# Kernel tuning notes

Hardware: AMD Instinct MI355X
Metric: run time of the kernel (lower is better)

Reference implementation:

```python
import jax, jax.numpy as jnp
import numpy as np

GRAPH_SIZE = 1024
D_MODEL = 256
BATCH = 32
INITIAL_ALPHA = 1.0


def setup_inputs() -> dict:
    key = jax.random.key(0)
    ks = jax.random.split(key, 10)
    s = 1.0 / np.sqrt(D_MODEL)  # torch Linear default init scale
    inp = {
        "query": jax.random.normal(ks[0], (BATCH, GRAPH_SIZE, D_MODEL), jnp.float32),
        "key_": jax.random.normal(ks[1], (BATCH, GRAPH_SIZE, D_MODEL), jnp.float32),
        "value": jax.random.normal(ks[2], (BATCH, GRAPH_SIZE, D_MODEL), jnp.float32),
        "dist": jax.random.uniform(ks[3], (BATCH, GRAPH_SIZE, GRAPH_SIZE), jnp.float32),
        "Wq": jax.random.uniform(ks[4], (D_MODEL, D_MODEL), jnp.float32, -s, s),
        "bq": jax.random.uniform(ks[5], (D_MODEL,), jnp.float32, -s, s),
        "Wk": jax.random.uniform(ks[6], (D_MODEL, D_MODEL), jnp.float32, -s, s),
        "bk": jax.random.uniform(ks[7], (D_MODEL,), jnp.float32, -s, s),
        "Wv": jax.random.uniform(ks[8], (D_MODEL, D_MODEL), jnp.float32, -s, s),
        "bv": jax.random.uniform(ks[9], (D_MODEL,), jnp.float32, -s, s),
        # alpha_raw = exp(initial_alpha - 1)
        "alpha_raw": jnp.asarray(np.exp(INITIAL_ALPHA - 1.0), jnp.float32),
    }
    return inp


def reference(query, key_, value, dist, Wq, bq, Wk, bk, Wv, bv, alpha_raw):
    # self-attention path: mask=None, cross=False, query_size == graph_size
    log2_N = jnp.log2(jnp.asarray(GRAPH_SIZE, jnp.float32))
    alpha = jax.nn.softplus(alpha_raw) + 1e-6

    q = jnp.einsum('bnd,ed->bne', query, Wq) + bq   # fc_q
    k = jnp.einsum('bnd,ed->bne', key_, Wk) + bk    # fc_k
    v = jnp.einsum('bnd,ed->bne', value, Wv) + bv   # fc_v

    exp_A = jnp.exp(-alpha * log2_N * dist)         # [b, n, n]
    exp_K = jnp.exp(k)                              # [b, n, d]

    numerator = jnp.einsum('bqk,bkd->bqd', exp_A, exp_K * v)
    denominator = jnp.einsum('bqk,bkd->bqd', exp_A, exp_K) + 1e-8
    return jax.nn.sigmoid(q) * (numerator / denominator)
```

## Files before the change

### kernel.cpp

```cpp
#include <hip/hip_runtime.h>
#include <hip/hip_bf16.h>

#define NBATCH 32
#define NG 1024
#define DM 256
#define HB 16

typedef short bf16x8 __attribute__((ext_vector_type(8)));
typedef float f32x4 __attribute__((ext_vector_type(4)));
typedef unsigned short u16x4 __attribute__((ext_vector_type(4)));
typedef unsigned short u16x8 __attribute__((ext_vector_type(8)));

static __device__ __forceinline__ unsigned short f2bf(float f) {
    __hip_bfloat16 h = __float2bfloat16(f);
    return *reinterpret_cast<unsigned short*>(&h);
}

static __device__ __forceinline__ void gload16(const void* g, void* l) {
    __builtin_amdgcn_global_load_lds(
        (const __attribute__((address_space(1))) unsigned int*)g,
        (__attribute__((address_space(3))) unsigned int*)l, 16, 0, 0);
}

__global__ __launch_bounds__(256) void wpack_kernel(
    const float* __restrict__ Wq, const float* __restrict__ Wk,
    const float* __restrict__ Wv, unsigned short* __restrict__ Wb)
{
    const int i4 = (blockIdx.x * 256 + threadIdx.x) * 4;
    const int t = i4 >> 16;
    const int off = i4 & 65535;
    const float* src = (t == 0) ? Wq : (t == 1) ? Wk : Wv;
    float4 v = *(const float4*)(src + off);
    *(u16x4*)(Wb + i4) = (u16x4){ f2bf(v.x), f2bf(v.y), f2bf(v.z), f2bf(v.w) };
}

__global__ __launch_bounds__(256) void conv_kernel(
    const float* __restrict__ src, unsigned short* __restrict__ dst)
{
    const size_t i8 = ((size_t)blockIdx.x * 256 + threadIdx.x) * 8;
    float4 a = *(const float4*)(src + i8);
    float4 b = *(const float4*)(src + i8 + 4);
    *(u16x8*)(dst + i8) = (u16x8){ f2bf(a.x), f2bf(a.y), f2bf(a.z), f2bf(a.w),
                                   f2bf(b.x), f2bf(b.y), f2bf(b.z), f2bf(b.w) };
}

__global__ __launch_bounds__(256) void projq_kernel(
    const unsigned short* __restrict__ Xq,
    const unsigned short* __restrict__ Wb,
    const float* __restrict__ bq,
    float* __restrict__ sigq)
{
    __shared__ __align__(128) unsigned short lds[2][2][128 * 64];

    const int bid = blockIdx.x;
    const int mt = bid >> 1, nt = bid & 1;
    const int tid = threadIdx.x;
    const int w = tid >> 6, lane = tid & 63;
    const int wm = w >> 1, wn = w & 1;
    const int l15 = lane & 15, lhi = lane >> 4;
    const int lr = lane >> 3, sl = lane & 7;
    const int sp = sl ^ lr;

    const char* Abase = (const char*)(Xq + (size_t)mt * 128 * 256);
    const char* Wbase = (const char*)(Wb + (size_t)nt * 128 * 256);

    f32x4 acc[4][4];
    #pragma unroll
    for (int mi = 0; mi < 4; ++mi)
        #pragma unroll
        for (int ni = 0; ni < 4; ++ni)
            acc[mi][ni] = (f32x4){0.f, 0.f, 0.f, 0.f};

    auto STAGE = [&](int buf, int t) {
        #pragma unroll
        for (int i = 0; i < 4; ++i) {
            const int r = w * 32 + i * 8 + lr;
            gload16(Abase + (size_t)r * 512 + t * 128 + sp * 16,
                    (char*)&lds[buf][0][0] + w * 4096 + i * 1024);
            gload16(Wbase + (size_t)r * 512 + t * 128 + sp * 16,
                    (char*)&lds[buf][1][0] + w * 4096 + i * 1024);
        }
    };

    STAGE(0, 0);
    __syncthreads();

    int cur = 0;
    for (int t = 0; t < 4; ++t) {
        if (t < 3) STAGE(cur ^ 1, t + 1);
        const char* Ab = (const char*)&lds[cur][0][0];
        const char* Bb = (const char*)&lds[cur][1][0];
        #pragma unroll
        for (int kk = 0; kk < 2; ++kk) {
            bf16x8 af[4], bfr[4];
            #pragma unroll
            for (int mi = 0; mi < 4; ++mi) {
                const int tr = wm * 64 + mi * 16 + l15;
                af[mi] = *(const bf16x8*)(Ab + ((tr * 128 + kk * 64 + lhi * 16) ^ ((tr & 7) << 4)));
            }
            #pragma unroll
            for (int ni = 0; ni < 4; ++ni) {
                const int tr = wn * 64 + ni * 16 + l15;
                bfr[ni] = *(const bf16x8*)(Bb + ((tr * 128 + kk * 64 + lhi * 16) ^ ((tr & 7) << 4)));
            }
            #pragma unroll
            for (int mi = 0; mi < 4; ++mi)
                #pragma unroll
                for (int ni = 0; ni < 4; ++ni)
                    acc[mi][ni] = __builtin_amdgcn_mfma_f32_16x16x32_bf16(
                        af[mi], bfr[ni], acc[mi][ni], 0, 0, 0);
        }
        __syncthreads();
        cur ^= 1;
    }

    #pragma unroll
    for (int ni = 0; ni < 4; ++ni) {
        const int c = nt * 128 + wn * 64 + ni * 16 + l15;
        const float bqs = bq[c];
        #pragma unroll
        for (int mi = 0; mi < 4; ++mi)
            #pragma unroll
            for (int r = 0; r < 4; ++r) {
                const size_t R = (size_t)mt * 128 + wm * 64 + mi * 16 + lhi * 4 + r;
                const float qv = acc[mi][ni][r] + bqs;
                sigq[R * DM + c] = 1.0f / (1.0f + __expf(-qv));
            }
    }
}

__global__ __launch_bounds__(256) void projkv_kernel(
    const unsigned short* __restrict__ Xk,
    const unsigned short* __restrict__ Xv,
    const unsigned short* __restrict__ Wkb,
    const unsigned short* __restrict__ Wvb,
    const float* __restrict__ bk, const float* __restrict__ bv,
    unsigned short* __restrict__ Pt)
{
    __shared__ __align__(128) unsigned short lds[2][2][128 * 64];

    const int bid = blockIdx.x;
    const int mt = bid >> 1, nt = bid & 1;
    const int tid = threadIdx.x;
    const int w = tid >> 6, lane = tid & 63;
    const int wm = w >> 1, wn = w & 1;
    const int l15 = lane & 15, lhi = lane >> 4;
    const int lr = lane >> 3, sl = lane & 7;
    const int sp = sl ^ lr;
    const int g16 = (sp & 3) * 16;

    f32x4 kacc[4][4], vacc[4][4];
    #pragma unroll
    for (int mi = 0; mi < 4; ++mi)
        #pragma unroll
        for (int ni = 0; ni < 4; ++ni) {
            kacc[mi][ni] = (f32x4){0.f, 0.f, 0.f, 0.f};
            vacc[mi][ni] = (f32x4){0.f, 0.f, 0.f, 0.f};
        }

    auto STAGE = [&](int buf, int t) {
        #pragma unroll
        for (int i = 0; i < 4; ++i) {
            const int r = w * 32 + i * 8 + lr;
            const char* asrc = (sp < 4 ? (const char*)Xk : (const char*)Xv)
                               + (size_t)(mt * 128 + r) * 512 + t * 64 + g16;
            gload16(asrc, (char*)&lds[buf][0][0] + w * 4096 + i * 1024);
            const char* wsrc = (sp < 4 ? (const char*)Wkb : (const char*)Wvb)
                               + (size_t)(nt * 128 + r) * 512 + t * 64 + g16;
            gload16(wsrc, (char*)&lds[buf][1][0] + w * 4096 + i * 1024);
        }
    };

    STAGE(0, 0);
    __syncthreads();

    int cur = 0;
    for (int t = 0; t < 8; ++t) {
        if (t < 7) STAGE(cur ^ 1, t + 1);
        const char* Ab = (const char*)&lds[cur][0][0];
        const char* Bb = (const char*)&lds[cur][1][0];
        bf16x8 kaf[4], vaf[4], kbf[4], vbf[4];
        #pragma unroll
        for (int mi = 0; mi < 4; ++mi) {
            const int tr = wm * 64 + mi * 16 + l15;
            const int sw = (tr & 7) << 4;
            kaf[mi] = *(const bf16x8*)(Ab + ((tr * 128 + lhi * 16) ^ sw));
            vaf[mi] = *(const bf16x8*)(Ab + ((tr * 128 + 64 + lhi * 16) ^ sw));
        }
        #pragma unroll
        for (int ni = 0; ni < 4; ++ni) {
            const int tr = wn * 64 + ni * 16 + l15;
            const int sw = (tr & 7) << 4;
            kbf[ni] = *(const bf16x8*)(Bb + ((tr * 128 + lhi * 16) ^ sw));
            vbf[ni] = *(const bf16x8*)(Bb + ((tr * 128 + 64 + lhi * 16) ^ sw));
        }
        #pragma unroll
        for (int mi = 0; mi < 4; ++mi)
            #pragma unroll
            for (int ni = 0; ni < 4; ++ni) {
                kacc[mi][ni] = __builtin_amdgcn_mfma_f32_16x16x32_bf16(
                    kaf[mi], kbf[ni], kacc[mi][ni], 0, 0, 0);
                vacc[mi][ni] = __builtin_amdgcn_mfma_f32_16x16x32_bf16(
                    vaf[mi], vbf[ni], vacc[mi][ni], 0, 0, 0);
            }
        __syncthreads();
        cur ^= 1;
    }

    const int b = (mt * 128) >> 10;
    const int kb0 = (mt * 128) & 1023;
    #pragma unroll
    for (int ni = 0; ni < 4; ++ni) {
        const int c = nt * 128 + wn * 64 + ni * 16 + l15;
        const float bks = bk[c], bvs = bv[c];
        #pragma unroll
        for (int mi = 0; mi < 4; ++mi) {
            unsigned short p1[4], p2[4];
            #pragma unroll
            for (int r = 0; r < 4; ++r) {
                const float ek = __expf(kacc[mi][ni][r] + bks);
                const float vv = vacc[mi][ni][r] + bvs;
                p1[r] = f2bf(ek * vv);
                p2[r] = f2bf(ek);
            }
            const int kidx = kb0 + wm * 64 + mi * 16 + lhi * 4;
            *(u16x4*)&Pt[((size_t)b * 512 + 2 * c    ) * NG + kidx] =
                (u16x4){p1[0], p1[1], p1[2], p1[3]};
            *(u16x4*)&Pt[((size_t)b * 512 + 2 * c + 1) * NG + kidx] =
                (u16x4){p2[0], p2[1], p2[2], p2[3]};
        }
    }
}

__global__ __launch_bounds__(256) void exp_kernel(
    const float* __restrict__ dist, unsigned short* __restrict__ ea,
    const float* __restrict__ alpha_raw)
{
    const float alpha = log1pf(__expf(alpha_raw[0])) + 1e-6f;
    const float sc = -alpha * 10.0f * 1.44269504088896f;
    const size_t i8 = ((size_t)blockIdx.x * 256 + threadIdx.x) * 8;
    float4 v0 = *(const float4*)(dist + i8);
    float4 v1 = *(const float4*)(dist + i8 + 4);
    u16x8 o = { f2bf(exp2f(sc * v0.x)), f2bf(exp2f(sc * v0.y)),
                f2bf(exp2f(sc * v0.z)), f2bf(exp2f(sc * v0.w)),
                f2bf(exp2f(sc * v1.x)), f2bf(exp2f(sc * v1.y)),
                f2bf(exp2f(sc * v1.z)), f2bf(exp2f(sc * v1.w)) };
    *(u16x8*)(ea + i8) = o;
}

__global__ __launch_bounds__(256) void attn_kernel(
    const unsigned short* __restrict__ ea,
    const unsigned short* __restrict__ Pt,
    float* __restrict__ out)
{
    __shared__ __align__(128) unsigned short lds[2][2][128 * 64];

    const int bid = blockIdx.x;
    const int l = (bid & 7) * 64 + (bid >> 3);
    const int b = l >> 5;
    const int m = (l >> 2) & 7;
    const int n = l & 3;

    const int tid = threadIdx.x;
    const int w = tid >> 6, lane = tid & 63;
    const int wm = w >> 1, wn = w & 1;
    const int l15 = lane & 15, lhi = lane >> 4;
    const int lr = lane >> 3, cb = lane & 7;
    const int cbs = cb ^ lr;

    const char* Abase = (const char*)(ea + ((size_t)b * NG + m * 128) * NG);
    const char* Bbase = (const char*)(Pt + ((size_t)b * 512 + n * 128) * NG);

    f32x4 acc[4][4];
    #pragma unroll
    for (int mi = 0; mi < 4; ++mi)
        #pragma unroll
        for (int ni = 0; ni < 4; ++ni)
            acc[mi][ni] = (f32x4){0.f, 0.f, 0.f, 0.f};

    auto STAGE = [&](int buf, int t) {
        #pragma unroll
        for (int i = 0; i < 4; ++i) {
            const int r = w * 32 + i * 8 + lr;
            const size_t goff = (size_t)r * 2048 + t * 128 + cbs * 16;
            char* ldst = (char*)&lds[buf][0][0] + w * 4096 + i * 1024;
            gload16(Abase + goff, ldst);
            gload16(Bbase + goff, ldst + 16384);
        }
    };

    STAGE(0, 0);
    __syncthreads();

    int cur = 0;
    for (int t = 0; t < 16; ++t) {
        if (t < 15) STAGE(cur ^ 1, t + 1);
        const char* Ab = (const char*)&lds[cur][0][0];
        const char* Bb = (const char*)&lds[cur][1][0];
        #pragma unroll
        for (int kk = 0; kk < 2; ++kk) {
            const int bc = kk * 64 + lhi * 16;
            bf16x8 af[4], bfr[4];
            #pragma unroll
            for (int mi = 0; mi < 4; ++mi) {
                const int tr = wm * 64 + mi * 16 + l15;
                af[mi] = *(const bf16x8*)(Ab + ((tr * 128 + bc) ^ ((tr & 7) << 4)));
            }
            #pragma unroll
            for (int ni = 0; ni < 4; ++ni) {
                const int tr = wn * 64 + ni * 16 + l15;
                bfr[ni] = *(const bf16x8*)(Bb + ((tr * 128 + bc) ^ ((tr & 7) << 4)));
            }
            #pragma unroll
            for (int mi = 0; mi < 4; ++mi)
                #pragma unroll
                for (int ni = 0; ni < 4; ++ni)
                    acc[mi][ni] = __builtin_amdgcn_mfma_f32_16x16x32_bf16(
                        af[mi], bfr[ni], acc[mi][ni], 0, 0, 0);
        }
        __syncthreads();
        cur ^= 1;
    }

    const int parity = lane & 1;
    #pragma unroll
    for (int mi = 0; mi < 4; ++mi)
        #pragma unroll
        for (int ni = 0; ni < 4; ++ni)
            #pragma unroll
            for (int r = 0; r < 4; ++r) {
                const float own = acc[mi][ni][r];
                const float other = __shfl_xor(own, 1, 64);
                if (!parity) {
                    const int colg = n * 128 + wn * 64 + ni * 16 + l15;
                    const int d = colg >> 1;
                    const int rowg = m * 128 + wm * 64 + mi * 16 + lhi * 4 + r;
                    const size_t idx = ((size_t)b * NG + rowg) * DM + d;
                    out[idx] = out[idx] * (own / (other + 1e-8f));
                }
            }
}

extern "C" void kernel_launch(void* const* d_in, const int* in_sizes, int n_in,
                              void* d_out, int out_size, void* d_ws, size_t ws_size,
                              hipStream_t stream) {
    const float* query = (const float*)d_in[0];
    const float* key_  = (const float*)d_in[1];
    const float* value = (const float*)d_in[2];
    const float* dist  = (const float*)d_in[3];
    const float* Wq = (const float*)d_in[4];
    const float* bq = (const float*)d_in[5];
    const float* Wk = (const float*)d_in[6];
    const float* bk = (const float*)d_in[7];
    const float* Wv = (const float*)d_in[8];
    const float* bv = (const float*)d_in[9];
    const float* alpha_raw = (const float*)d_in[10];
    float* out = (float*)d_out;

    unsigned short* Pt = (unsigned short*)d_ws;
    unsigned short* exp_buf =
        (unsigned short*)((char*)d_ws + (size_t)NBATCH * 512 * NG * sizeof(unsigned short));
    unsigned short* Wb = exp_buf + (size_t)HB * NG * NG;

    const size_t XN = (size_t)NBATCH * NG * DM;

    wpack_kernel<<<dim3(192), dim3(256), 0, stream>>>(Wq, Wk, Wv, Wb);

    conv_kernel<<<dim3(4096), dim3(256), 0, stream>>>(query, exp_buf);
    projq_kernel<<<dim3(512), dim3(256), 0, stream>>>(exp_buf, Wb, bq, out);

    unsigned short* Xk = exp_buf;
    unsigned short* Xv = exp_buf + XN;
    conv_kernel<<<dim3(4096), dim3(256), 0, stream>>>(key_, Xk);
    conv_kernel<<<dim3(4096), dim3(256), 0, stream>>>(value, Xv);
    projkv_kernel<<<dim3(512), dim3(256), 0, stream>>>(
        Xk, Xv, Wb + 65536, Wb + 131072, bk, bv, Pt);

    for (int h = 0; h < 2; ++h) {
        exp_kernel<<<dim3(8192), dim3(256), 0, stream>>>(
            dist + (size_t)h * HB * NG * NG, exp_buf, alpha_raw);
        attn_kernel<<<dim3(512), dim3(256), 0, stream>>>(
            exp_buf, Pt + (size_t)h * HB * 512 * NG, out + (size_t)h * HB * NG * DM);
    }
}
```

Before: 194.5 us.

## Fuse dist exponentiation into attention kernel and merge input conversions

The separate exp_kernel, which wrote a bf16 exp(-alpha*log2N*dist) buffer to memory, is removed. The attention kernel now loads fp32 dist tiles into registers, computes the exponential and bf16 conversion itself, and writes the result to LDS, overlapping this with the MFMA loop. This avoids the bf16 write and re-read of the large [B,N,N] intermediate, and a single 1024-block attention launch replaces two half-batch passes. The three input conversion kernels are also merged into one launch. In exchange, the attention kernel reads fp32 dist (twice the bytes of bf16) and carries extra register pressure for the staged float4 values.

After: 244.2 us. 25.6% more time.

```diff
diff --git a/kernel.cpp b/kernel.cpp
--- a/kernel.cpp
+++ b/kernel.cpp
@@ -4,7 +4,6 @@
 #define NBATCH 32
 #define NG 1024
 #define DM 256
-#define HB 16
 
 typedef short bf16x8 __attribute__((ext_vector_type(8)));
 typedef float f32x4 __attribute__((ext_vector_type(4)));
@@ -34,14 +33,18 @@
     *(u16x4*)(Wb + i4) = (u16x4){ f2bf(v.x), f2bf(v.y), f2bf(v.z), f2bf(v.w) };
 }
 
-__global__ __launch_bounds__(256) void conv_kernel(
-    const float* __restrict__ src, unsigned short* __restrict__ dst)
-{
-    const size_t i8 = ((size_t)blockIdx.x * 256 + threadIdx.x) * 8;
+__global__ __launch_bounds__(256) void conv3_kernel(
+    const float* __restrict__ q, const float* __restrict__ k,
+    const float* __restrict__ v, unsigned short* __restrict__ Xb)
+{
+    const int sel = blockIdx.x >> 12;
+    const float* src = (sel == 0) ? q : (sel == 1) ? k : v;
+    const size_t i8 = (((size_t)(blockIdx.x & 4095)) * 256 + threadIdx.x) * 8;
     float4 a = *(const float4*)(src + i8);
     float4 b = *(const float4*)(src + i8 + 4);
-    *(u16x8*)(dst + i8) = (u16x8){ f2bf(a.x), f2bf(a.y), f2bf(a.z), f2bf(a.w),
-                                   f2bf(b.x), f2bf(b.y), f2bf(b.z), f2bf(b.w) };
+    *(u16x8*)(Xb + (size_t)sel * NBATCH * NG * DM + i8) =
+        (u16x8){ f2bf(a.x), f2bf(a.y), f2bf(a.z), f2bf(a.w),
+                 f2bf(b.x), f2bf(b.y), f2bf(b.z), f2bf(b.w) };
 }
 
 __global__ __launch_bounds__(256) void projq_kernel(
@@ -232,31 +235,15 @@
     }
 }
 
-__global__ __launch_bounds__(256) void exp_kernel(
-    const float* __restrict__ dist, unsigned short* __restrict__ ea,
-    const float* __restrict__ alpha_raw)
-{
-    const float alpha = log1pf(__expf(alpha_raw[0])) + 1e-6f;
-    const float sc = -alpha * 10.0f * 1.44269504088896f;
-    const size_t i8 = ((size_t)blockIdx.x * 256 + threadIdx.x) * 8;
-    float4 v0 = *(const float4*)(dist + i8);
-    float4 v1 = *(const float4*)(dist + i8 + 4);
-    u16x8 o = { f2bf(exp2f(sc * v0.x)), f2bf(exp2f(sc * v0.y)),
-                f2bf(exp2f(sc * v0.z)), f2bf(exp2f(sc * v0.w)),
-                f2bf(exp2f(sc * v1.x)), f2bf(exp2f(sc * v1.y)),
-                f2bf(exp2f(sc * v1.z)), f2bf(exp2f(sc * v1.w)) };
-    *(u16x8*)(ea + i8) = o;
-}
-
 __global__ __launch_bounds__(256) void attn_kernel(
-    const unsigned short* __restrict__ ea,
-    const unsigned short* __restrict__ Pt,
-    float* __restrict__ out)
-{
-    __shared__ __align__(128) unsigned short lds[2][2][128 * 64];
+    const float* __restrict__ dist, const unsigned short* __restrict__ Pt,
+    const float* __restrict__ alpha_raw, float* __restrict__ out)
+{
+    __shared__ __align__(128) unsigned short lds_a[2][128 * 64];
+    __shared__ __align__(128) unsigned short lds_b[2][128 * 64];
 
     const int bid = blockIdx.x;
-    const int l = (bid & 7) * 64 + (bid >> 3);
+    const int l = (bid & 7) * 128 + (bid >> 3);
     const int b = l >> 5;
     const int m = (l >> 2) & 7;
     const int n = l & 3;
@@ -268,7 +255,11 @@
     const int lr = lane >> 3, cb = lane & 7;
     const int cbs = cb ^ lr;
 
-    const char* Abase = (const char*)(ea + ((size_t)b * NG + m * 128) * NG);
+    const float alpha = log1pf(__expf(alpha_raw[0])) + 1e-6f;
+    const float sc = -alpha * 10.0f * 1.44269504088896f;
+
+    const int sr = tid >> 1, scol = (tid & 1) << 5;
+    const float* dbase = dist + ((size_t)b * NG + m * 128 + sr) * NG + scol;
     const char* Bbase = (const char*)(Pt + ((size_t)b * 512 + n * 128) * NG);
 
     f32x4 acc[4][4];
@@ -278,25 +269,46 @@
         for (int ni = 0; ni < 4; ++ni)
             acc[mi][ni] = (f32x4){0.f, 0.f, 0.f, 0.f};
 
-    auto STAGE = [&](int buf, int t) {
+    float4 fr[8];
+    auto ALOAD = [&](int t) {
+        #pragma unroll
+        for (int j = 0; j < 8; ++j)
+            fr[j] = *(const float4*)(dbase + t * 64 + 4 * j);
+    };
+    auto AWRITE = [&](int buf) {
+        char* base = (char*)&lds_a[buf][0];
+        #pragma unroll
+        for (int j = 0; j < 4; ++j) {
+            float4 a = fr[2 * j], c = fr[2 * j + 1];
+            u16x8 p = { f2bf(exp2f(sc * a.x)), f2bf(exp2f(sc * a.y)),
+                        f2bf(exp2f(sc * a.z)), f2bf(exp2f(sc * a.w)),
+                        f2bf(exp2f(sc * c.x)), f2bf(exp2f(sc * c.y)),
+                        f2bf(exp2f(sc * c.z)), f2bf(exp2f(sc * c.w)) };
+            *(u16x8*)(base + ((sr * 128 + scol * 2 + 16 * j) ^ ((sr & 7) << 4))) = p;
+        }
+    };
+    auto BSTAGE = [&](int buf, int t) {
         #pragma unroll
         for (int i = 0; i < 4; ++i) {
             const int r = w * 32 + i * 8 + lr;
-            const size_t goff = (size_t)r * 2048 + t * 128 + cbs * 16;
-            char* ldst = (char*)&lds[buf][0][0] + w * 4096 + i * 1024;
-            gload16(Abase + goff, ldst);
-            gload16(Bbase + goff, ldst + 16384);
-        }
-    };
-
-    STAGE(0, 0);
+            gload16(Bbase + (size_t)r * 2048 + t * 128 + cbs * 16,
+                    (char*)&lds_b[buf][0] + w * 4096 + i * 1024);
+        }
+    };
+
+    ALOAD(0);
+    BSTAGE(0, 0);
+    AWRITE(0);
     __syncthreads();
 
     int cur = 0;
     for (int t = 0; t < 16; ++t) {
-        if (t < 15) STAGE(cur ^ 1, t + 1);
-        const char* Ab = (const char*)&lds[cur][0][0];
-        const char* Bb = (const char*)&lds[cur][1][0];
+        if (t < 15) {
+            ALOAD(t + 1);
+            BSTAGE(cur ^ 1, t + 1);
+        }
+        const char* Ab = (const char*)&lds_a[cur][0];
+        const char* Bb = (const char*)&lds_b[cur][0];
         #pragma unroll
         for (int kk = 0; kk < 2; ++kk) {
             const int bc = kk * 64 + lhi * 16;
@@ -318,6 +330,7 @@
                     acc[mi][ni] = __builtin_amdgcn_mfma_f32_16x16x32_bf16(
                         af[mi], bfr[ni], acc[mi][ni], 0, 0, 0);
         }
+        if (t < 15) AWRITE(cur ^ 1);
         __syncthreads();
         cur ^= 1;
     }
@@ -358,28 +371,16 @@
     float* out = (float*)d_out;
 
     unsigned short* Pt = (unsigned short*)d_ws;
-    unsigned short* exp_buf =
-        (unsigned short*)((char*)d_ws + (size_t)NBATCH * 512 * NG * sizeof(unsigned short));
-    unsigned short* Wb = exp_buf + (size_t)HB * NG * NG;
-
+    unsigned short* Xb = Pt + (size_t)NBATCH * 512 * NG;
     const size_t XN = (size_t)NBATCH * NG * DM;
+    unsigned short* Wb = Xb + 3 * XN;
 
     wpack_kernel<<<dim3(192), dim3(256), 0, stream>>>(Wq, Wk, Wv, Wb);
-
-    conv_kernel<<<dim3(4096), dim3(256), 0, stream>>>(query, exp_buf);
-    projq_kernel<<<dim3(512), dim3(256), 0, stream>>>(exp_buf, Wb, bq, out);
-
-    unsigned short* Xk = exp_buf;
-    unsigned short* Xv = exp_buf + XN;
-    conv_kernel<<<dim3(4096), dim3(256), 0, stream>>>(key_, Xk);
-    conv_kernel<<<dim3(4096), dim3(256), 0, stream>>>(value, Xv);
+    conv3_kernel<<<dim3(12288), dim3(256), 0, stream>>>(query, key_, value, Xb);
+
+    projq_kernel<<<dim3(512), dim3(256), 0, stream>>>(Xb, Wb, bq, out);
     projkv_kernel<<<dim3(512), dim3(256), 0, stream>>>(
-        Xk, Xv, Wb + 65536, Wb + 131072, bk, bv, Pt);
-
-    for (int h = 0; h < 2; ++h) {
-        exp_kernel<<<dim3(8192), dim3(256), 0, stream>>>(
-            dist + (size_t)h * HB * NG * NG, exp_buf, alpha_raw);
-        attn_kernel<<<dim3(512), dim3(256), 0, stream>>>(
-            exp_buf, Pt + (size_t)h * HB * 512 * NG, out + (size_t)h * HB * NG * DM);
-    }
-}
+        Xb + XN, Xb + 2 * XN, Wb + 65536, Wb + 131072, bk, bv, Pt);
+
+    attn_kernel<<<dim3(1024), dim3(256), 0, stream>>>(dist, Pt, alpha_raw, out);
+}
```

## Single-buffer GEMM LDS, merge conversions, run exp and attention over whole batch

Applied to the files above, without the earlier changes.

Drops LDS double-buffering in the projection and attention GEMMs, going to load-sync-compute-sync with half the shared memory per block, which may allow more resident blocks. The three fp32-to-bf16 conversions are merged into one launch. The exp and attention kernels now each run once over all 32 batches with a full-size workspace instead of in two halves, and the attention block-index mapping is updated to match. This cuts launches and raises occupancy, but gives up overlap of global loads with MFMA inside a block and needs a larger workspace.

Result: slower. 208.4 us (+7.2%).

```diff
diff --git a/kernel.cpp b/kernel.cpp
--- a/kernel.cpp
+++ b/kernel.cpp
@@ -4,7 +4,6 @@
 #define NBATCH 32
 #define NG 1024
 #define DM 256
-#define HB 16
 
 typedef short bf16x8 __attribute__((ext_vector_type(8)));
 typedef float f32x4 __attribute__((ext_vector_type(4)));
@@ -34,202 +33,18 @@
     *(u16x4*)(Wb + i4) = (u16x4){ f2bf(v.x), f2bf(v.y), f2bf(v.z), f2bf(v.w) };
 }
 
-__global__ __launch_bounds__(256) void conv_kernel(
-    const float* __restrict__ src, unsigned short* __restrict__ dst)
-{
-    const size_t i8 = ((size_t)blockIdx.x * 256 + threadIdx.x) * 8;
+__global__ __launch_bounds__(256) void conv3_kernel(
+    const float* __restrict__ q, const float* __restrict__ k,
+    const float* __restrict__ v, unsigned short* __restrict__ Xb)
+{
+    const int sel = blockIdx.x >> 12;
+    const float* src = (sel == 0) ? q : (sel == 1) ? k : v;
+    const size_t i8 = (((size_t)(blockIdx.x & 4095)) * 256 + threadIdx.x) * 8;
     float4 a = *(const float4*)(src + i8);
     float4 b = *(const float4*)(src + i8 + 4);
-    *(u16x8*)(dst + i8) = (u16x8){ f2bf(a.x), f2bf(a.y), f2bf(a.z), f2bf(a.w),
-                                   f2bf(b.x), f2bf(b.y), f2bf(b.z), f2bf(b.w) };
-}
-
-__global__ __launch_bounds__(256) void projq_kernel(
-    const unsigned short* __restrict__ Xq,
-    const unsigned short* __restrict__ Wb,
-    const float* __restrict__ bq,
-    float* __restrict__ sigq)
-{
-    __shared__ __align__(128) unsigned short lds[2][2][128 * 64];
-
-    const int bid = blockIdx.x;
-    const int mt = bid >> 1, nt = bid & 1;
-    const int tid = threadIdx.x;
-    const int w = tid >> 6, lane = tid & 63;
-    const int wm = w >> 1, wn = w & 1;
-    const int l15 = lane & 15, lhi = lane >> 4;
-    const int lr = lane >> 3, sl = lane & 7;
-    const int sp = sl ^ lr;
-
-    const char* Abase = (const char*)(Xq + (size_t)mt * 128 * 256);
-    const char* Wbase = (const char*)(Wb + (size_t)nt * 128 * 256);
-
-    f32x4 acc[4][4];
-    #pragma unroll
-    for (int mi = 0; mi < 4; ++mi)
-        #pragma unroll
-        for (int ni = 0; ni < 4; ++ni)
-            acc[mi][ni] = (f32x4){0.f, 0.f, 0.f, 0.f};
-
-    auto STAGE = [&](int buf, int t) {
-        #pragma unroll
-        for (int i = 0; i < 4; ++i) {
-            const int r = w * 32 + i * 8 + lr;
-            gload16(Abase + (size_t)r * 512 + t * 128 + sp * 16,
-                    (char*)&lds[buf][0][0] + w * 4096 + i * 1024);
-            gload16(Wbase + (size_t)r * 512 + t * 128 + sp * 16,
-                    (char*)&lds[buf][1][0] + w * 4096 + i * 1024);
-        }
-    };
-
-    STAGE(0, 0);
-    __syncthreads();
-
-    int cur = 0;
-    for (int t = 0; t < 4; ++t) {
-        if (t < 3) STAGE(cur ^ 1, t + 1);
-        const char* Ab = (const char*)&lds[cur][0][0];
-        const char* Bb = (const char*)&lds[cur][1][0];
-        #pragma unroll
-        for (int kk = 0; kk < 2; ++kk) {
-            bf16x8 af[4], bfr[4];
-            #pragma unroll
-            for (int mi = 0; mi < 4; ++mi) {
-                const int tr = wm * 64 + mi * 16 + l15;
-                af[mi] = *(const bf16x8*)(Ab + ((tr * 128 + kk * 64 + lhi * 16) ^ ((tr & 7) << 4)));
-            }
-            #pragma unroll
-            for (int ni = 0; ni < 4; ++ni) {
-                const int tr = wn * 64 + ni * 16 + l15;
-                bfr[ni] = *(const bf16x8*)(Bb + ((tr * 128 + kk * 64 + lhi * 16) ^ ((tr & 7) << 4)));
-            }
-            #pragma unroll
-            for (int mi = 0; mi < 4; ++mi)
-                #pragma unroll
-                for (int ni = 0; ni < 4; ++ni)
-                    acc[mi][ni] = __builtin_amdgcn_mfma_f32_16x16x32_bf16(
-                        af[mi], bfr[ni], acc[mi][ni], 0, 0, 0);
-        }
-        __syncthreads();
-        cur ^= 1;
-    }
-
-    #pragma unroll
-    for (int ni = 0; ni < 4; ++ni) {
-        const int c = nt * 128 + wn * 64 + ni * 16 + l15;
-        const float bqs = bq[c];
-        #pragma unroll
-        for (int mi = 0; mi < 4; ++mi)
-            #pragma unroll
-            for (int r = 0; r < 4; ++r) {
-                const size_t R = (size_t)mt * 128 + wm * 64 + mi * 16 + lhi * 4 + r;
-                const float qv = acc[mi][ni][r] + bqs;
-                sigq[R * DM + c] = 1.0f / (1.0f + __expf(-qv));
-            }
-    }
-}
-
-__global__ __launch_bounds__(256) void projkv_kernel(
-    const unsigned short* __restrict__ Xk,
-    const unsigned short* __restrict__ Xv,
-    const unsigned short* __restrict__ Wkb,
-    const unsigned short* __restrict__ Wvb,
-    const float* __restrict__ bk, const float* __restrict__ bv,
-    unsigned short* __restrict__ Pt)
-{
-    __shared__ __align__(128) unsigned short lds[2][2][128 * 64];
-
-    const int bid = blockIdx.x;
-    const int mt = bid >> 1, nt = bid & 1;
-    const int tid = threadIdx.x;
-    const int w = tid >> 6, lane = tid & 63;
-    const int wm = w >> 1, wn = w & 1;
-    const int l15 = lane & 15, lhi = lane >> 4;
-    const int lr = lane >> 3, sl = lane & 7;
-    const int sp = sl ^ lr;
-    const int g16 = (sp & 3) * 16;
-
-    f32x4 kacc[4][4], vacc[4][4];
-    #pragma unroll
-    for (int mi = 0; mi < 4; ++mi)
-        #pragma unroll
-        for (int ni = 0; ni < 4; ++ni) {
-            kacc[mi][ni] = (f32x4){0.f, 0.f, 0.f, 0.f};
-            vacc[mi][ni] = (f32x4){0.f, 0.f, 0.f, 0.f};
-        }
-
-    auto STAGE = [&](int buf, int t) {
-        #pragma unroll
-        for (int i = 0; i < 4; ++i) {
-            const int r = w * 32 + i * 8 + lr;
-            const char* asrc = (sp < 4 ? (const char*)Xk : (const char*)Xv)
-                               + (size_t)(mt * 128 + r) * 512 + t * 64 + g16;
-            gload16(asrc, (char*)&lds[buf][0][0] + w * 4096 + i * 1024);
-            const char* wsrc = (sp < 4 ? (const char*)Wkb : (const char*)Wvb)
-                               + (size_t)(nt * 128 + r) * 512 + t * 64 + g16;
-            gload16(wsrc, (char*)&lds[buf][1][0] + w * 4096 + i * 1024);
-        }
-    };
-
-    STAGE(0, 0);
-    __syncthreads();
-
-    int cur = 0;
-    for (int t = 0; t < 8; ++t) {
-        if (t < 7) STAGE(cur ^ 1, t + 1);
-        const char* Ab = (const char*)&lds[cur][0][0];
-        const char* Bb = (const char*)&lds[cur][1][0];
-        bf16x8 kaf[4], vaf[4], kbf[4], vbf[4];
-        #pragma unroll
-        for (int mi = 0; mi < 4; ++mi) {
-            const int tr = wm * 64 + mi * 16 + l15;
-            const int sw = (tr & 7) << 4;
-            kaf[mi] = *(const bf16x8*)(Ab + ((tr * 128 + lhi * 16) ^ sw));
-            vaf[mi] = *(const bf16x8*)(Ab + ((tr * 128 + 64 + lhi * 16) ^ sw));
-        }
-        #pragma unroll
-        for (int ni = 0; ni < 4; ++ni) {
-            const int tr = wn * 64 + ni * 16 + l15;
-            const int sw = (tr & 7) << 4;
-            kbf[ni] = *(const bf16x8*)(Bb + ((tr * 128 + lhi * 16) ^ sw));
-            vbf[ni] = *(const bf16x8*)(Bb + ((tr * 128 + 64 + lhi * 16) ^ sw));
-        }
-        #pragma unroll
-        for (int mi = 0; mi < 4; ++mi)
-            #pragma unroll
-            for (int ni = 0; ni < 4; ++ni) {
-                kacc[mi][ni] = __builtin_amdgcn_mfma_f32_16x16x32_bf16(
-                    kaf[mi], kbf[ni], kacc[mi][ni], 0, 0, 0);
-                vacc[mi][ni] = __builtin_amdgcn_mfma_f32_16x16x32_bf16(
-                    vaf[mi], vbf[ni], vacc[mi][ni], 0, 0, 0);
-            }
-        __syncthreads();
-        cur ^= 1;
-    }
-
-    const int b = (mt * 128) >> 10;
-    const int kb0 = (mt * 128) & 1023;
-    #pragma unroll
-    for (int ni = 0; ni < 4; ++ni) {
-        const int c = nt * 128 + wn * 64 + ni * 16 + l15;
-        const float bks = bk[c], bvs = bv[c];
-        #pragma unroll
-        for (int mi = 0; mi < 4; ++mi) {
-            unsigned short p1[4], p2[4];
-            #pragma unroll
-            for (int r = 0; r < 4; ++r) {
-                const float ek = __expf(kacc[mi][ni][r] + bks);
-                const float vv = vacc[mi][ni][r] + bvs;
-                p1[r] = f2bf(ek * vv);
-                p2[r] = f2bf(ek);
-            }
-            const int kidx = kb0 + wm * 64 + mi * 16 + lhi * 4;
-            *(u16x4*)&Pt[((size_t)b * 512 + 2 * c    ) * NG + kidx] =
-                (u16x4){p1[0], p1[1], p1[2], p1[3]};
-            *(u16x4*)&Pt[((size_t)b * 512 + 2 * c + 1) * NG + kidx] =
-                (u16x4){p2[0], p2[1], p2[2], p2[3]};
-        }
-    }
+    *(u16x8*)(Xb + (size_t)sel * NBATCH * NG * DM + i8) =
+        (u16x8){ f2bf(a.x), f2bf(a.y), f2bf(a.z), f2bf(a.w),
+                 f2bf(b.x), f2bf(b.y), f2bf(b.z), f2bf(b.w) };
 }
 
 __global__ __launch_bounds__(256) void exp_kernel(
@@ -248,15 +63,188 @@
     *(u16x8*)(ea + i8) = o;
 }
 
+__global__ __launch_bounds__(256) void projq_kernel(
+    const unsigned short* __restrict__ Xq,
+    const unsigned short* __restrict__ Wb,
+    const float* __restrict__ bq,
+    float* __restrict__ sigq)
+{
+    __shared__ __align__(128) unsigned short lds_a[128 * 64];
+    __shared__ __align__(128) unsigned short lds_b[128 * 64];
+
+    const int bid = blockIdx.x;
+    const int mt = bid >> 1, nt = bid & 1;
+    const int tid = threadIdx.x;
+    const int w = tid >> 6, lane = tid & 63;
+    const int wm = w >> 1, wn = w & 1;
+    const int l15 = lane & 15, lhi = lane >> 4;
+    const int lr = lane >> 3, sl = lane & 7;
+    const int sp = sl ^ lr;
+
+    const char* Abase = (const char*)(Xq + (size_t)mt * 128 * 256);
+    const char* Wbase = (const char*)(Wb + (size_t)nt * 128 * 256);
+
+    f32x4 acc[4][4];
+    #pragma unroll
+    for (int mi = 0; mi < 4; ++mi)
+        #pragma unroll
+        for (int ni = 0; ni < 4; ++ni)
+            acc[mi][ni] = (f32x4){0.f, 0.f, 0.f, 0.f};
+
+    for (int t = 0; t < 4; ++t) {
+        #pragma unroll
+        for (int i = 0; i < 4; ++i) {
+            const int r = w * 32 + i * 8 + lr;
+            gload16(Abase + (size_t)r * 512 + t * 128 + sp * 16,
+                    (char*)lds_a + w * 4096 + i * 1024);
+            gload16(Wbase + (size_t)r * 512 + t * 128 + sp * 16,
+                    (char*)lds_b + w * 4096 + i * 1024);
+        }
+        __syncthreads();
+        #pragma unroll
+        for (int kk = 0; kk < 2; ++kk) {
+            bf16x8 af[4], bfr[4];
+            #pragma unroll
+            for (int mi = 0; mi < 4; ++mi) {
+                const int tr = wm * 64 + mi * 16 + l15;
+                af[mi] = *(const bf16x8*)((const char*)lds_a +
+                         ((tr * 128 + kk * 64 + lhi * 16) ^ ((tr & 7) << 4)));
+            }
+            #pragma unroll
+            for (int ni = 0; ni < 4; ++ni) {
+                const int tr = wn * 64 + ni * 16 + l15;
+                bfr[ni] = *(const bf16x8*)((const char*)lds_b +
+                          ((tr * 128 + kk * 64 + lhi * 16) ^ ((tr & 7) << 4)));
+            }
+            #pragma unroll
+            for (int mi = 0; mi < 4; ++mi)
+                #pragma unroll
+                for (int ni = 0; ni < 4; ++ni)
+                    acc[mi][ni] = __builtin_amdgcn_mfma_f32_16x16x32_bf16(
+                        af[mi], bfr[ni], acc[mi][ni], 0, 0, 0);
+        }
+        __syncthreads();
+    }
+
+    #pragma unroll
+    for (int ni = 0; ni < 4; ++ni) {
+        const int c = nt * 128 + wn * 64 + ni * 16 + l15;
+        const float bqs = bq[c];
+        #pragma unroll
+        for (int mi = 0; mi < 4; ++mi)
+            #pragma unroll
+            for (int r = 0; r < 4; ++r) {
+                const size_t R = (size_t)mt * 128 + wm * 64 + mi * 16 + lhi * 4 + r;
+                const float qv = acc[mi][ni][r] + bqs;
+                sigq[R * DM + c] = 1.0f / (1.0f + __expf(-qv));
+            }
+    }
+}
+
+__global__ __launch_bounds__(256) void projkv_kernel(
+    const unsigned short* __restrict__ Xk,
+    const unsigned short* __restrict__ Xv,
+    const unsigned short* __restrict__ Wkb,
+    const unsigned short* __restrict__ Wvb,
+    const float* __restrict__ bk, const float* __restrict__ bv,
+    unsigned short* __restrict__ Pt)
+{
+    __shared__ __align__(128) unsigned short lds_a[128 * 64];
+    __shared__ __align__(128) unsigned short lds_b[128 * 64];
+
+    const int bid = blockIdx.x;
+    const int mt = bid >> 1, nt = bid & 1;
+    const int tid = threadIdx.x;
+    const int w = tid >> 6, lane = tid & 63;
+    const int wm = w >> 1, wn = w & 1;
+    const int l15 = lane & 15, lhi = lane >> 4;
+    const int lr = lane >> 3, sl = lane & 7;
+    const int sp = sl ^ lr;
+    const int g16 = (sp & 3) * 16;
+
+    f32x4 kacc[4][4], vacc[4][4];
+    #pragma unroll
+    for (int mi = 0; mi < 4; ++mi)
+        #pragma unroll
+        for (int ni = 0; ni < 4; ++ni) {
+            kacc[mi][ni] = (f32x4){0.f, 0.f, 0.f, 0.f};
+            vacc[mi][ni] = (f32x4){0.f, 0.f, 0.f, 0.f};
+        }
+
+    for (int t = 0; t < 8; ++t) {
+        #pragma unroll
+        for (int i = 0; i < 4; ++i) {
+            const int r = w * 32 + i * 8 + lr;
+            const char* asrc = (sp < 4 ? (const char*)Xk : (const char*)Xv)
+                               + (size_t)(mt * 128 + r) * 512 + t * 64 + g16;
+            gload16(asrc, (char*)lds_a + w * 4096 + i * 1024);
+            const char* wsrc = (sp < 4 ? (const char*)Wkb : (const char*)Wvb)
+                               + (size_t)(nt * 128 + r) * 512 + t * 64 + g16;
+            gload16(wsrc, (char*)lds_b + w * 4096 + i * 1024);
+        }
+        __syncthreads();
+        bf16x8 kaf[4], vaf[4], kbf[4], vbf[4];
+        #pragma unroll
+        for (int mi = 0; mi < 4; ++mi) {
+            const int tr = wm * 64 + mi * 16 + l15;
+            const int sw = (tr & 7) << 4;
+            kaf[mi] = *(const bf16x8*)((const char*)lds_a + ((tr * 128 + lhi * 16) ^ sw));
+            vaf[mi] = *(const bf16x8*)((const char*)lds_a + ((tr * 128 + 64 + lhi * 16) ^ sw));
+        }
+        #pragma unroll
+        for (int ni = 0; ni < 4; ++ni) {
+            const int tr = wn * 64 + ni * 16 + l15;
+            const int sw = (tr & 7) << 4;
+            kbf[ni] = *(const bf16x8*)((const char*)lds_b + ((tr * 128 + lhi * 16) ^ sw));
+            vbf[ni] = *(const bf16x8*)((const char*)lds_b + ((tr * 128 + 64 + lhi * 16) ^ sw));
+        }
+        #pragma unroll
+        for (int mi = 0; mi < 4; ++mi)
+            #pragma unroll
+            for (int ni = 0; ni < 4; ++ni) {
+                kacc[mi][ni] = __builtin_amdgcn_mfma_f32_16x16x32_bf16(
+                    kaf[mi], kbf[ni], kacc[mi][ni], 0, 0, 0);
+                vacc[mi][ni] = __builtin_amdgcn_mfma_f32_16x16x32_bf16(
+                    vaf[mi], vbf[ni], vacc[mi][ni], 0, 0, 0);
+            }
+        __syncthreads();
+    }
+
+    const int b = (mt * 128) >> 10;
+    const int kb0 = (mt * 128) & 1023;
+    #pragma unroll
+    for (int ni = 0; ni < 4; ++ni) {
+        const int c = nt * 128 + wn * 64 + ni * 16 + l15;
+        const float bks = bk[c], bvs = bv[c];
+        #pragma unroll
+        for (int mi = 0; mi < 4; ++mi) {
+            unsigned short p1[4], p2[4];
+            #pragma unroll
+            for (int r = 0; r < 4; ++r) {
+                const float ek = __expf(kacc[mi][ni][r] + bks);
+                const float vv = vacc[mi][ni][r] + bvs;
+                p1[r] = f2bf(ek * vv);
+                p2[r] = f2bf(ek);
+            }
+            const int kidx = kb0 + wm * 64 + mi * 16 + lhi * 4;
+            *(u16x4*)&Pt[((size_t)b * 512 + 2 * c    ) * NG + kidx] =
+                (u16x4){p1[0], p1[1], p1[2], p1[3]};
+            *(u16x4*)&Pt[((size_t)b * 512 + 2 * c + 1) * NG + kidx] =
+                (u16x4){p2[0], p2[1], p2[2], p2[3]};
+        }
+    }
+}
+
 __global__ __launch_bounds__(256) void attn_kernel(
     const unsigned short* __restrict__ ea,
     const unsigned short* __restrict__ Pt,
     float* __restrict__ out)
 {
-    __shared__ __align__(128) unsigned short lds[2][2][128 * 64];
+    __shared__ __align__(128) unsigned short lds_a[128 * 64];
+    __shared__ __align__(128) unsigned short lds_b[128 * 64];
 
     const int bid = blockIdx.x;
-    const int l = (bid & 7) * 64 + (bid >> 3);
+    const int l = (bid & 7) * 128 + (bid >> 3);
     const int b = l >> 5;
     const int m = (l >> 2) & 7;
     const int n = l & 3;
@@ -278,25 +266,15 @@
         for (int ni = 0; ni < 4; ++ni)
             acc[mi][ni] = (f32x4){0.f, 0.f, 0.f, 0.f};
 
-    auto STAGE = [&](int buf, int t) {
+    for (int t = 0; t < 16; ++t) {
         #pragma unroll
         for (int i = 0; i < 4; ++i) {
             const int r = w * 32 + i * 8 + lr;
             const size_t goff = (size_t)r * 2048 + t * 128 + cbs * 16;
-            char* ldst = (char*)&lds[buf][0][0] + w * 4096 + i * 1024;
-            gload16(Abase + goff, ldst);
-            gload16(Bbase + goff, ldst + 16384);
-        }
-    };
-
-    STAGE(0, 0);
-    __syncthreads();
-
-    int cur = 0;
-    for (int t = 0; t < 16; ++t) {
-        if (t < 15) STAGE(cur ^ 1, t + 1);
-        const char* Ab = (const char*)&lds[cur][0][0];
-        const char* Bb = (const char*)&lds[cur][1][0];
+            gload16(Abase + goff, (char*)lds_a + w * 4096 + i * 1024);
+            gload16(Bbase + goff, (char*)lds_b + w * 4096 + i * 1024);
+        }
+        __syncthreads();
         #pragma unroll
         for (int kk = 0; kk < 2; ++kk) {
             const int bc = kk * 64 + lhi * 16;
@@ -304,12 +282,14 @@
             #pragma unroll
             for (int mi = 0; mi < 4; ++mi) {
                 const int tr = wm * 64 + mi * 16 + l15;
-                af[mi] = *(const bf16x8*)(Ab + ((tr * 128 + bc) ^ ((tr & 7) << 4)));
+                af[mi] = *(const bf16x8*)((const char*)lds_a +
+                         ((tr * 128 + bc) ^ ((tr & 7) << 4)));
             }
             #pragma unroll
             for (int ni = 0; ni < 4; ++ni) {
                 const int tr = wn * 64 + ni * 16 + l15;
-                bfr[ni] = *(const bf16x8*)(Bb + ((tr * 128 + bc) ^ ((tr & 7) << 4)));
+                bfr[ni] = *(const bf16x8*)((const char*)lds_b +
+                          ((tr * 128 + bc) ^ ((tr & 7) << 4)));
             }
             #pragma unroll
             for (int mi = 0; mi < 4; ++mi)
@@ -319,7 +299,6 @@
                         af[mi], bfr[ni], acc[mi][ni], 0, 0, 0);
         }
         __syncthreads();
-        cur ^= 1;
     }
 
     const int parity = lane & 1;
@@ -358,28 +337,18 @@
     float* out = (float*)d_out;
 
     unsigned short* Pt = (unsigned short*)d_ws;
-    unsigned short* exp_buf =
-        (unsigned short*)((char*)d_ws + (size_t)NBATCH * 512 * NG * sizeof(unsigned short));
-    unsigned short* Wb = exp_buf + (size_t)HB * NG * NG;
-
+    unsigned short* ea = Pt + (size_t)NBATCH * 512 * NG;
+    unsigned short* Xb = ea + (size_t)NBATCH * NG * NG;
     const size_t XN = (size_t)NBATCH * NG * DM;
+    unsigned short* Wb = Xb + 3 * XN;
 
     wpack_kernel<<<dim3(192), dim3(256), 0, stream>>>(Wq, Wk, Wv, Wb);
-
-    conv_kernel<<<dim3(4096), dim3(256), 0, stream>>>(query, exp_buf);
-    projq_kernel<<<dim3(512), dim3(256), 0, stream>>>(exp_buf, Wb, bq, out);
-
-    unsigned short* Xk = exp_buf;
-    unsigned short* Xv = exp_buf + XN;
-    conv_kernel<<<dim3(4096), dim3(256), 0, stream>>>(key_, Xk);
-    conv_kernel<<<dim3(4096), dim3(256), 0, stream>>>(value, Xv);
+    conv3_kernel<<<dim3(12288), dim3(256), 0, stream>>>(query, key_, value, Xb);
+
+    projq_kernel<<<dim3(512), dim3(256), 0, stream>>>(Xb, Wb, bq, out);
     projkv_kernel<<<dim3(512), dim3(256), 0, stream>>>(
-        Xk, Xv, Wb + 65536, Wb + 131072, bk, bv, Pt);
-
-    for (int h = 0; h < 2; ++h) {
-        exp_kernel<<<dim3(8192), dim3(256), 0, stream>>>(
-            dist + (size_t)h * HB * NG * NG, exp_buf, alpha_raw);
-        attn_kernel<<<dim3(512), dim3(256), 0, stream>>>(
-            exp_buf, Pt + (size_t)h * HB * 512 * NG, out + (size_t)h * HB * NG * DM);
-    }
-}
+        Xb + XN, Xb + 2 * XN, Wb + 65536, Wb + 131072, bk, bv, Pt);
+
+    exp_kernel<<<dim3(16384), dim3(256), 0, stream>>>(dist, ea, alpha_raw);
+    attn_kernel<<<dim3(1024), dim3(256), 0, stream>>>(ea, Pt, out);
+}
```
